# Kernel tuning notes

Hardware: AMD Instinct MI355X
Metric: run time of the kernel (lower is better)

The kernel has to match this reference:

```python
import jax, jax.numpy as jnp
import numpy as np

N_NODES = 100000
NEG_SLOPE = 0.2


def gat_conv(x, W, att_src, att_dst, bias, src, dst, heads, out_ch):
    # x: [N, F_in]; W: [F_in, heads*out_ch]; att_*: [heads, out_ch]; bias: [heads*out_ch]
    N = x.shape[0]
    h = (x @ W).reshape(N, heads, out_ch)                 # [N, H, C]
    a_src = jnp.sum(h * att_src[None], axis=-1)           # [N, H]
    a_dst = jnp.sum(h * att_dst[None], axis=-1)           # [N, H]
    # per-edge unnormalized attention logits (PyG GATConv)
    alpha = jax.nn.leaky_relu(a_src[src] + a_dst[dst], NEG_SLOPE)   # [E, H]
    # scatter-softmax over edges grouped by destination node
    m = jax.ops.segment_max(alpha, dst, num_segments=N)   # [N, H]
    m = jnp.where(jnp.isfinite(m), m, 0.0)
    e = jnp.exp(alpha - m[dst])                           # [E, H]
    s = jax.ops.segment_sum(e, dst, num_segments=N)       # [N, H]
    alpha = e / (s[dst] + 1e-16)
    # weighted scatter-add aggregation of neighbor features
    out = jax.ops.segment_sum(alpha[:, :, None] * h[src], dst, num_segments=N)  # [N, H, C]
    return out.reshape(N, heads * out_ch) + bias


def setup_inputs() -> dict:
    key = jax.random.key(0)
    ks = jax.random.split(key, 10)
    F_in = 128
    x = jax.random.normal(ks[0], (N_NODES, F_in), dtype=jnp.float32)
    edge_index = jax.random.randint(ks[1], (2, 3200000), 0, N_NODES, dtype=jnp.int64)
    g = 0.1
    return {
        "x": x,
        "edge_index": edge_index,
        "W1": jax.random.normal(ks[2], (F_in, 32), jnp.float32) * g,
        "att_src1": jax.random.normal(ks[3], (2, 16), jnp.float32) * g,
        "att_dst1": jax.random.normal(ks[4], (2, 16), jnp.float32) * g,
        "b1": jnp.zeros((32,), jnp.float32),
        "W2": jax.random.normal(ks[5], (32, 2), jnp.float32) * g,
        "att_src2": jax.random.normal(ks[6], (1, 2), jnp.float32) * g,
        "att_dst2": jax.random.normal(ks[7], (1, 2), jnp.float32) * g,
        "b2": jnp.zeros((2,), jnp.float32),
    }


def reference(x, edge_index, W1, att_src1, att_dst1, b1, W2, att_src2, att_dst2, b2):
    N = x.shape[0]
    # add self-loops (PyG GATConv default add_self_loops=True)
    loops = jnp.arange(N, dtype=edge_index.dtype)
    src = jnp.concatenate([edge_index[0], loops])
    dst = jnp.concatenate([edge_index[1], loops])
    h = gat_conv(x, W1, att_src1, att_dst1, b1, src, dst, heads=2, out_ch=16)
    h = jax.nn.elu(h)
    h = gat_conv(h, W2, att_src2, att_dst2, b2, src, dst, heads=1, out_ch=2)
    return jax.nn.log_softmax(h, axis=1)
```

## Files before the change

### kernel.cpp

```cpp
#include <hip/hip_runtime.h>
#include <hip/hip_bf16.h>
#include <hip/hip_fp16.h>

#define LEAK   0.2f
#define NPB    200
#define CAP    8192
#define CAPSH  13
#define SBITS  17
#define SMASK  0x1FFFF
#define CHUNKB 8192

__device__ __forceinline__ unsigned pkh(float a, float b) {
    __half2 h = __floats2half2_rn(a, b);
    return *(unsigned*)&h;
}
__device__ __forceinline__ float2 uph(unsigned u) {
    __half2 h = *(__half2*)&u;
    return __half22float2(h);
}

__global__ __launch_bounds__(512) void kpre(const int* __restrict__ ei, int E, int K,
                                            int NBIN,
                                            int* __restrict__ cursor,
                                            int* __restrict__ binned,
                                            const float* __restrict__ x,
                                            const float* __restrict__ W1,
                                            const float* __restrict__ atts,
                                            const float* __restrict__ attd,
                                            uint2* __restrict__ h1h,
                                            float* __restrict__ a1s,
                                            float* __restrict__ a1d, int N) {
    __shared__ __align__(16) char smem[57380];
    int t = threadIdx.x;

    if (blockIdx.x < NBIN) {
        int* hist = (int*)smem;
        int* gb    = hist + 512;
        int* lbase = gb + 512;
        int* lcur  = lbase + 512;
        unsigned short* rbk = (unsigned short*)(lcur + 512);
        int* sv    = (int*)(rbk + CHUNKB);
        int* swt   = sv + CHUNKB;
        int* probe = swt + 8;
        hist[t] = 0;
        if (t == 0) *probe = 0;
        __syncthreads();
        if (t < 256) {
            int zc = 0;
#pragma unroll
            for (int j = 0; j < 4; j++) zc += (ei[(t * 4 + j) * 2 + 1] == 0) ? 1 : 0;
            if (zc) atomicAdd(probe, zc);
        }
        __syncthreads();
        int f = (*probe == 1024);
        int e0 = blockIdx.x * CHUNKB;
        int ss[16], dd[16];
#pragma unroll
        for (int i = 0; i < 16; i++) {
            int e = e0 + t + 512 * i;
            ss[i] = -1;
            dd[i] = 0;
            if (e < E) {
                int s, d;
                if (f) { s = ei[2 * e]; d = ei[2 * (e + E)]; }
                else   { s = ei[e];     d = ei[e + E]; }
                ss[i] = s;
                dd[i] = d;
                atomicAdd(&hist[d / NPB], 1);
            }
        }
        __syncthreads();
        int h = (t < K) ? hist[t] : 0;
        if (h) gb[t] = (t << CAPSH) + atomicAdd(&cursor[t], h);
        int xsc = h;
#pragma unroll
        for (int o = 1; o < 64; o <<= 1) {
            int y = __shfl_up(xsc, o, 64);
            if ((t & 63) >= o) xsc += y;
        }
        if ((t & 63) == 63) swt[t >> 6] = xsc;
        __syncthreads();
        int add = 0;
#pragma unroll
        for (int j = 0; j < 8; j++)
            if (j < (t >> 6)) add += swt[j];
        int lb = xsc - h + add;
        lbase[t] = lb;
        lcur[t] = lb;
        __syncthreads();
#pragma unroll
        for (int i = 0; i < 16; i++) {
            if (ss[i] >= 0) {
                int bk = dd[i] / NPB;
                int dloc = dd[i] - bk * NPB;
                int pos = atomicAdd(&lcur[bk], 1);
                sv[pos] = ss[i] | (dloc << SBITS);
                rbk[pos] = (unsigned short)bk;
            }
        }
        __syncthreads();
        int tot = min(CHUNKB, E - e0);
        for (int i = t; i < tot; i += 512) {
            int bk = rbk[i];
            int gpos = gb[bk] + (i - lbase[bk]);
            if (gpos < ((bk + 1) << CAPSH))
                binned[gpos] = sv[i];
        }
    } else {
        int b = blockIdx.x - NBIN;
        float* Ws = (float*)smem;
        float* xs = Ws + 4096;
        const float4* W4 = (const float4*)W1;
        float4* Ws4 = (float4*)Ws;
#pragma unroll
        for (int i = 0; i < 2; i++) Ws4[t + 512 * i] = W4[t + 512 * i];
        long long node0 = (long long)b * 64;
        const float4* x4 = (const float4*)x;
        float4* xs4 = (float4*)xs;
#pragma unroll
        for (int i = 0; i < 4; i++) {
            int idx = t + 512 * i;
            int row = idx >> 5, col = idx & 31;
            long long n = node0 + row;
            float4 v = make_float4(0.f, 0.f, 0.f, 0.f);
            if (n < N) v = x4[n * 32 + col];
            xs4[row * 33 + col] = v;
        }
        __syncthreads();

        int cg = t & 7, ns = t >> 3;
        const float4* xr = (const float4*)(xs + ns * 132);
        float acc[4] = {0.f, 0.f, 0.f, 0.f};
#pragma unroll 8
        for (int k4 = 0; k4 < 32; k4++) {
            float4 xa = xr[k4];
            float av[4] = {xa.x, xa.y, xa.z, xa.w};
#pragma unroll
            for (int i = 0; i < 4; i++) {
                float4 w = Ws4[(k4 * 4 + i) * 8 + cg];
                acc[0] = fmaf(av[i], w.x, acc[0]);
                acc[1] = fmaf(av[i], w.y, acc[1]);
                acc[2] = fmaf(av[i], w.z, acc[2]);
                acc[3] = fmaf(av[i], w.w, acc[3]);
            }
        }
        long long gn = node0 + ns;
        if (gn < N) h1h[gn * 8 + cg] = make_uint2(pkh(acc[0], acc[1]),
                                                  pkh(acc[2], acc[3]));
        float ps = 0.f, pd = 0.f;
#pragma unroll
        for (int i = 0; i < 4; i++) {
            ps = fmaf(acc[i], atts[cg * 4 + i], ps);
            pd = fmaf(acc[i], attd[cg * 4 + i], pd);
        }
#pragma unroll
        for (int m = 1; m < 4; m <<= 1) {
            ps += __shfl_xor(ps, m, 64);
            pd += __shfl_xor(pd, m, 64);
        }
        if ((cg & 3) == 0) {
            int hd = cg >> 2;
            if (gn < N) { a1s[gn * 2 + hd] = ps; a1d[gn * 2 + hd] = pd; }
        }
    }
}

__global__ __launch_bounds__(1024) void kfused(const int* __restrict__ cursor,
                                               const int* __restrict__ binned,
                                               const uint2* __restrict__ h1h,
                                               const float* __restrict__ a1s,
                                               const float* __restrict__ a1d,
                                               const float* __restrict__ b1,
                                               const float* __restrict__ W2,
                                               const float* __restrict__ as2,
                                               const float* __restrict__ ad2,
                                               float4* __restrict__ pk,
                                               int* __restrict__ srcs,
                                               int* __restrict__ od, int N) {
    __shared__ int lsrc[CAP];
    __shared__ int ldeg[NPB], lcur[NPB], loff[NPB];
    __shared__ int swt[4];
    int b = blockIdx.x, t = threadIdx.x;
    int node0 = b * NPB;
    int nn = min(NPB, N - node0);
    int cnt = cursor[b];
    if (cnt > CAP) cnt = CAP;
    const int* bb = binned + ((long long)b << CAPSH);
    if (t < NPB) ldeg[t] = 0;
    __syncthreads();
    int pv[8];
#pragma unroll
    for (int j = 0; j < 8; j++) {
        int i = t + 1024 * j;
        pv[j] = (i < cnt) ? bb[i] : -1;
        if (pv[j] >= 0) atomicAdd(&ldeg[pv[j] >> SBITS], 1);
    }
    __syncthreads();
    {
        int v = 0, xsc = 0;
        if (t < 256) {
            v = (t < nn) ? ldeg[t] : 0;
            xsc = v;
#pragma unroll
            for (int o = 1; o < 64; o <<= 1) {
                int y = __shfl_up(xsc, o, 64);
                if ((t & 63) >= o) xsc += y;
            }
            if ((t & 63) == 63) swt[t >> 6] = xsc;
        }
        __syncthreads();
        if (t < 256) {
            int add = 0;
#pragma unroll
            for (int j = 0; j < 4; j++)
                if (j < (t >> 6)) add += swt[j];
            xsc += add;
            if (t < nn) {
                int rel = xsc - v;
                loff[t] = rel;
                lcur[t] = rel;
                od[node0 + t] = rel | (v << 14);
            }
        }
        __syncthreads();
    }
#pragma unroll
    for (int j = 0; j < 8; j++) {
        if (pv[j] >= 0) {
            int pos = atomicAdd(&lcur[pv[j] >> SBITS], 1);
            lsrc[pos] = pv[j] & SMASK;
        }
    }
    __syncthreads();
    for (int i = t; i < cnt; i += 1024) srcs[((long long)b << CAPSH) + i] = lsrc[i];

    int wv = t >> 6, lane = t & 63;
    int e8 = lane >> 3, c4 = lane & 7, hd = c4 >> 2;
    bool wlane = (c4 & 3) == 0;
    for (int ni = wv; ni < nn; ni += 16) {
        int n = node0 + ni;
        float a1dn = a1d[2 * n + hd];
        int base = loff[ni], g = ldeg[ni];
        float4 acc = make_float4(0.f, 0.f, 0.f, 0.f);
        float wsum = 0.f;
        for (int tt = e8 - 1; tt < g; tt += 16) {
            int t2 = tt + 8;
            bool p2 = t2 < g;
            int s0 = (tt < 0) ? n : lsrc[base + tt];
            int s1 = p2 ? lsrc[base + t2] : s0;
            float as0 = a1s[2 * s0 + hd];
            float as1 = a1s[2 * s1 + hd];
            uint2 hb0 = h1h[(size_t)s0 * 8 + c4];
            uint2 hb1 = h1h[(size_t)s1 * 8 + c4];
            float al0 = as0 + a1dn;
            al0 = al0 > 0.f ? al0 : LEAK * al0;
            float w0 = __expf(al0);
            float al1 = as1 + a1dn;
            al1 = al1 > 0.f ? al1 : LEAK * al1;
            float w1 = p2 ? __expf(al1) : 0.f;
            float2 f01 = uph(hb0.x), f23 = uph(hb0.y);
            float2 g01 = uph(hb1.x), g23 = uph(hb1.y);
            acc.x = fmaf(w0, f01.x, acc.x);
            acc.y = fmaf(w0, f01.y, acc.y);
            acc.z = fmaf(w0, f23.x, acc.z);
            acc.w = fmaf(w0, f23.y, acc.w);
            acc.x = fmaf(w1, g01.x, acc.x);
            acc.y = fmaf(w1, g01.y, acc.y);
            acc.z = fmaf(w1, g23.x, acc.z);
            acc.w = fmaf(w1, g23.y, acc.w);
            if (wlane) wsum += w0 + w1;
        }
#pragma unroll
        for (int m = 8; m < 64; m <<= 1) {
            acc.x += __shfl_xor(acc.x, m, 64);
            acc.y += __shfl_xor(acc.y, m, 64);
            acc.z += __shfl_xor(acc.z, m, 64);
            acc.w += __shfl_xor(acc.w, m, 64);
            wsum += __shfl_xor(wsum, m, 64);
        }
        float wsH = __shfl(wsum, hd * 4, 64);
        float inv = 1.f / (wsH + 1e-16f);
        float4 bv = ((const float4*)b1)[c4];
        float4 t1;
        t1.x = acc.x * inv + bv.x;
        t1.y = acc.y * inv + bv.y;
        t1.z = acc.z * inv + bv.z;
        t1.w = acc.w * inv + bv.w;
        t1.x = t1.x > 0.f ? t1.x : __expf(t1.x) - 1.f;
        t1.y = t1.y > 0.f ? t1.y : __expf(t1.y) - 1.f;
        t1.z = t1.z > 0.f ? t1.z : __expf(t1.z) - 1.f;
        t1.w = t1.w > 0.f ? t1.w : __expf(t1.w) - 1.f;
        const float4* W24 = (const float4*)W2;
        float4 wA = W24[c4 * 2], wB = W24[c4 * 2 + 1];
        float p0 = t1.x * wA.x + t1.y * wA.z + t1.z * wB.x + t1.w * wB.z;
        float p1 = t1.x * wA.y + t1.y * wA.w + t1.z * wB.y + t1.w * wB.w;
#pragma unroll
        for (int m = 1; m < 8; m <<= 1) {
            p0 += __shfl_xor(p0, m, 64);
            p1 += __shfl_xor(p1, m, 64);
        }
        if (lane == 0)
            pk[n] = make_float4(p0 * as2[0] + p1 * as2[1], p0, p1,
                                p0 * ad2[0] + p1 * ad2[1]);
    }
}

__global__ __launch_bounds__(256) void kagg2(const int* __restrict__ od,
                                             const int* __restrict__ srcs,
                                             const float4* __restrict__ pk,
                                             const float* __restrict__ b2,
                                             float* __restrict__ out, int N) {
    int sub = threadIdx.x >> 2, k = threadIdx.x & 3;
    int n = blockIdx.x * 64 + sub;
    if (n >= N) return;
    float4 pn = pk[n];
    float adn = pn.w;
    int o = od[n];
    int base = ((n / NPB) << CAPSH) + (o & 16383);
    int g = o >> 14;
    float a0 = 0.f, a1v = 0.f, wsm = 0.f;
    for (int e0 = k - 1; e0 < g; e0 += 32) {
        int ee[8];
        bool qq[8];
        int sS[8];
#pragma unroll
        for (int j = 0; j < 8; j++) {
            ee[j] = e0 + 4 * j;
            qq[j] = ee[j] < g;
        }
        sS[0] = (e0 < 0) ? n : srcs[base + e0];
#pragma unroll
        for (int j = 1; j < 8; j++) sS[j] = qq[j] ? srcs[base + ee[j]] : sS[0];
        float4 pp[8];
        pp[0] = (e0 < 0) ? pn : pk[sS[0]];
#pragma unroll
        for (int j = 1; j < 8; j++) pp[j] = pk[sS[j]];
#pragma unroll
        for (int j = 0; j < 8; j++) {
            float al = pp[j].x + adn;
            al = al > 0.f ? al : LEAK * al;
            float w = (j == 0 || qq[j]) ? __expf(al) : 0.f;
            a0  = fmaf(w, pp[j].y, a0);
            a1v = fmaf(w, pp[j].z, a1v);
            wsm += w;
        }
    }
#pragma unroll
    for (int m = 1; m < 4; m <<= 1) {
        a0 += __shfl_xor(a0, m, 64);
        a1v += __shfl_xor(a1v, m, 64);
        wsm += __shfl_xor(wsm, m, 64);
    }
    if (k == 0) {
        float inv = 1.f / (wsm + 1e-16f);
        float o0 = a0 * inv + b2[0];
        float o1 = a1v * inv + b2[1];
        float mx = fmaxf(o0, o1);
        float lse = mx + __logf(__expf(o0 - mx) + __expf(o1 - mx));
        ((float2*)out)[n] = make_float2(o0 - lse, o1 - lse);
    }
}

extern "C" void kernel_launch(void* const* d_in, const int* in_sizes, int n_in,
                              void* d_out, int out_size, void* d_ws, size_t ws_size,
                              hipStream_t stream) {
    const float* x   = (const float*)d_in[0];
    const int*   ei  = (const int*)d_in[1];
    const float* W1  = (const float*)d_in[2];
    const float* as1 = (const float*)d_in[3];
    const float* ad1 = (const float*)d_in[4];
    const float* b1  = (const float*)d_in[5];
    const float* W2  = (const float*)d_in[6];
    const float* as2 = (const float*)d_in[7];
    const float* ad2 = (const float*)d_in[8];
    const float* b2  = (const float*)d_in[9];
    float* out = (float*)d_out;

    int N = out_size / 2;
    int E = in_sizes[1] / 2;
    int K = (N + NPB - 1) / NPB;

    float* wsp   = (float*)d_ws;
    float4* pk   = (float4*)wsp;
    uint2* h1h   = (uint2*)(pk + (size_t)N);
    float* a1s   = (float*)(h1h + (size_t)N * 8);
    float* a1d   = a1s + (size_t)N * 2;
    int* od      = (int*)(a1d + (size_t)N * 2);
    int* srcs    = od + N;
    int* binned  = srcs + (size_t)K * CAP;
    int* cursor  = binned + (size_t)K * CAP;

    int NBIN = (E + CHUNKB - 1) / CHUNKB;
    int NK1  = (N + 63) / 64;

    hipMemsetAsync(cursor, 0, K * sizeof(int), stream);
    kpre<<<NBIN + NK1, 512, 0, stream>>>(ei, E, K, NBIN, cursor, binned,
                                         x, W1, as1, ad1, h1h, a1s, a1d, N);
    kfused<<<K, 1024, 0, stream>>>(cursor, binned, h1h, a1s, a1d,
                                   b1, W2, as2, ad2, pk, srcs, od, N);
    kagg2<<<(N + 63) / 64, 256, 0, stream>>>(od, srcs, pk, b2, out, N);
}
```

Baseline: 217.5 us.

## Split layer-1 features per head and aggregate heads in separate passes

Stores the half-precision layer-1 features as two per-head arrays (32 bytes per node each) and runs the edge aggregation once per head in two passes, staging partial sums in shared memory before the ELU/W2 epilogue. Each pass gathers a smaller per-node footprint, so the random-access working set per pass is halved and is more likely to stay in cache. In exchange, every edge's source index and a1s value is read twice, two extra block barriers are added, and each block uses more shared memory.

```diff
diff --git a/kernel.cpp b/kernel.cpp
--- a/kernel.cpp
+++ b/kernel.cpp
@@ -27,7 +27,8 @@
                                             const float* __restrict__ W1,
                                             const float* __restrict__ atts,
                                             const float* __restrict__ attd,
-                                            uint2* __restrict__ h1h,
+                                            uint2* __restrict__ h1a,
+                                            uint2* __restrict__ h1b,
                                             float* __restrict__ a1s,
                                             float* __restrict__ a1d, int N) {
     __shared__ __align__(16) char smem[57380];
@@ -145,8 +146,11 @@
             }
         }
         long long gn = node0 + ns;
-        if (gn < N) h1h[gn * 8 + cg] = make_uint2(pkh(acc[0], acc[1]),
-                                                  pkh(acc[2], acc[3]));
+        if (gn < N) {
+            uint2 v = make_uint2(pkh(acc[0], acc[1]), pkh(acc[2], acc[3]));
+            if (cg < 4) h1a[gn * 4 + cg] = v;
+            else        h1b[gn * 4 + (cg - 4)] = v;
+        }
         float ps = 0.f, pd = 0.f;
 #pragma unroll
         for (int i = 0; i < 4; i++) {
@@ -167,7 +171,8 @@
 
 __global__ __launch_bounds__(1024) void kfused(const int* __restrict__ cursor,
                                                const int* __restrict__ binned,
-                                               const uint2* __restrict__ h1h,
+                                               const uint2* __restrict__ h1a,
+                                               const uint2* __restrict__ h1b,
                                                const float* __restrict__ a1s,
                                                const float* __restrict__ a1d,
                                                const float* __restrict__ b1,
@@ -180,6 +185,7 @@
     __shared__ int lsrc[CAP];
     __shared__ int ldeg[NPB], lcur[NPB], loff[NPB];
     __shared__ int swt[4];
+    __shared__ float accS[NPB][36];
     int b = blockIdx.x, t = threadIdx.x;
     int node0 = b * NPB;
     int nn = min(NPB, N - node0);
@@ -235,57 +241,84 @@
     for (int i = t; i < cnt; i += 1024) srcs[((long long)b << CAPSH) + i] = lsrc[i];
 
     int wv = t >> 6, lane = t & 63;
-    int e8 = lane >> 3, c4 = lane & 7, hd = c4 >> 2;
-    bool wlane = (c4 & 3) == 0;
+    int e16 = lane >> 2, c2 = lane & 3;
+
     for (int ni = wv; ni < nn; ni += 16) {
         int n = node0 + ni;
-        float a1dn = a1d[2 * n + hd];
+        float a1dn = a1d[2 * n];
         int base = loff[ni], g = ldeg[ni];
         float4 acc = make_float4(0.f, 0.f, 0.f, 0.f);
         float wsum = 0.f;
-        for (int tt = e8 - 1; tt < g; tt += 16) {
-            int t2 = tt + 8;
-            bool p2 = t2 < g;
-            int s0 = (tt < 0) ? n : lsrc[base + tt];
-            int s1 = p2 ? lsrc[base + t2] : s0;
-            float as0 = a1s[2 * s0 + hd];
-            float as1 = a1s[2 * s1 + hd];
-            uint2 hb0 = h1h[(size_t)s0 * 8 + c4];
-            uint2 hb1 = h1h[(size_t)s1 * 8 + c4];
-            float al0 = as0 + a1dn;
-            al0 = al0 > 0.f ? al0 : LEAK * al0;
-            float w0 = __expf(al0);
-            float al1 = as1 + a1dn;
-            al1 = al1 > 0.f ? al1 : LEAK * al1;
-            float w1 = p2 ? __expf(al1) : 0.f;
-            float2 f01 = uph(hb0.x), f23 = uph(hb0.y);
-            float2 g01 = uph(hb1.x), g23 = uph(hb1.y);
-            acc.x = fmaf(w0, f01.x, acc.x);
-            acc.y = fmaf(w0, f01.y, acc.y);
-            acc.z = fmaf(w0, f23.x, acc.z);
-            acc.w = fmaf(w0, f23.y, acc.w);
-            acc.x = fmaf(w1, g01.x, acc.x);
-            acc.y = fmaf(w1, g01.y, acc.y);
-            acc.z = fmaf(w1, g23.x, acc.z);
-            acc.w = fmaf(w1, g23.y, acc.w);
-            if (wlane) wsum += w0 + w1;
-        }
-#pragma unroll
-        for (int m = 8; m < 64; m <<= 1) {
+        for (int tt = e16 - 1; tt < g; tt += 16) {
+            int s = (tt < 0) ? n : lsrc[base + tt];
+            float al = a1s[2 * s] + a1dn;
+            al = al > 0.f ? al : LEAK * al;
+            float w = __expf(al);
+            uint2 hb = h1a[(size_t)s * 4 + c2];
+            float2 f01 = uph(hb.x), f23 = uph(hb.y);
+            acc.x = fmaf(w, f01.x, acc.x);
+            acc.y = fmaf(w, f01.y, acc.y);
+            acc.z = fmaf(w, f23.x, acc.z);
+            acc.w = fmaf(w, f23.y, acc.w);
+            wsum += w;
+        }
+#pragma unroll
+        for (int m = 4; m < 64; m <<= 1) {
             acc.x += __shfl_xor(acc.x, m, 64);
             acc.y += __shfl_xor(acc.y, m, 64);
             acc.z += __shfl_xor(acc.z, m, 64);
             acc.w += __shfl_xor(acc.w, m, 64);
             wsum += __shfl_xor(wsum, m, 64);
         }
-        float wsH = __shfl(wsum, hd * 4, 64);
+        if (lane < 4) *(float4*)&accS[ni][c2 * 4] = acc;
+        if (lane == 0) accS[ni][32] = wsum;
+    }
+    __syncthreads();
+
+    for (int ni = wv; ni < nn; ni += 16) {
+        int n = node0 + ni;
+        float a1dn = a1d[2 * n + 1];
+        int base = loff[ni], g = ldeg[ni];
+        float4 acc = make_float4(0.f, 0.f, 0.f, 0.f);
+        float wsum = 0.f;
+        for (int tt = e16 - 1; tt < g; tt += 16) {
+            int s = (tt < 0) ? n : lsrc[base + tt];
+            float al = a1s[2 * s + 1] + a1dn;
+            al = al > 0.f ? al : LEAK * al;
+            float w = __expf(al);
+            uint2 hb = h1b[(size_t)s * 4 + c2];
+            float2 f01 = uph(hb.x), f23 = uph(hb.y);
+            acc.x = fmaf(w, f01.x, acc.x);
+            acc.y = fmaf(w, f01.y, acc.y);
+            acc.z = fmaf(w, f23.x, acc.z);
+            acc.w = fmaf(w, f23.y, acc.w);
+            wsum += w;
+        }
+#pragma unroll
+        for (int m = 4; m < 64; m <<= 1) {
+            acc.x += __shfl_xor(acc.x, m, 64);
+            acc.y += __shfl_xor(acc.y, m, 64);
+            acc.z += __shfl_xor(acc.z, m, 64);
+            acc.w += __shfl_xor(acc.w, m, 64);
+            wsum += __shfl_xor(wsum, m, 64);
+        }
+        if (lane < 4) *(float4*)&accS[ni][16 + c2 * 4] = acc;
+        if (lane == 0) accS[ni][33] = wsum;
+    }
+    __syncthreads();
+
+    int c4 = lane & 7, hd = c4 >> 2;
+    for (int ni = wv; ni < nn; ni += 16) {
+        int n = node0 + ni;
+        float4 accv = *(float4*)&accS[ni][c4 * 4];
+        float wsH = accS[ni][32 + hd];
         float inv = 1.f / (wsH + 1e-16f);
         float4 bv = ((const float4*)b1)[c4];
         float4 t1;
-        t1.x = acc.x * inv + bv.x;
-        t1.y = acc.y * inv + bv.y;
-        t1.z = acc.z * inv + bv.z;
-        t1.w = acc.w * inv + bv.w;
+        t1.x = accv.x * inv + bv.x;
+        t1.y = accv.y * inv + bv.y;
+        t1.z = accv.z * inv + bv.z;
+        t1.w = accv.w * inv + bv.w;
         t1.x = t1.x > 0.f ? t1.x : __expf(t1.x) - 1.f;
         t1.y = t1.y > 0.f ? t1.y : __expf(t1.y) - 1.f;
         t1.z = t1.z > 0.f ? t1.z : __expf(t1.z) - 1.f;
@@ -382,8 +415,9 @@
 
     float* wsp   = (float*)d_ws;
     float4* pk   = (float4*)wsp;
-    uint2* h1h   = (uint2*)(pk + (size_t)N);
-    float* a1s   = (float*)(h1h + (size_t)N * 8);
+    uint2* h1a   = (uint2*)(pk + (size_t)N);
+    uint2* h1b   = h1a + (size_t)N * 4;
+    float* a1s   = (float*)(h1b + (size_t)N * 4);
     float* a1d   = a1s + (size_t)N * 2;
     int* od      = (int*)(a1d + (size_t)N * 2);
     int* srcs    = od + N;
@@ -395,8 +429,8 @@
 
     hipMemsetAsync(cursor, 0, K * sizeof(int), stream);
     kpre<<<NBIN + NK1, 512, 0, stream>>>(ei, E, K, NBIN, cursor, binned,
-                                         x, W1, as1, ad1, h1h, a1s, a1d, N);
-    kfused<<<K, 1024, 0, stream>>>(cursor, binned, h1h, a1s, a1d,
+                                         x, W1, as1, ad1, h1a, h1b, a1s, a1d, N);
+    kfused<<<K, 1024, 0, stream>>>(cursor, binned, h1a, h1b, a1s, a1d,
                                    b1, W2, as2, ad2, pk, srcs, od, N);
     kagg2<<<(N + 63) / 64, 256, 0, stream>>>(od, srcs, pk, b2, out, N);
 }
```

New measurement: 247.8 us. 1.14x slower.
